# Kernel tuning notes

Measured on AMD Instinct MI355X. Metric: run time of the kernel, lower is better.

## Reference

```python
import jax, jax.numpy as jnp
import numpy as np

NUM_NODE = 90
FEAT_DIM = 32
BATCH = 8192


def setup_inputs() -> dict:
    key = jax.random.key(0)
    k1, k2, k3 = jax.random.split(key, 3)
    sc_feats = jax.random.normal(k1, (BATCH * NUM_NODE, FEAT_DIM), dtype=jnp.float32)
    fc_feats = jax.random.normal(k2, (BATCH * NUM_NODE, FEAT_DIM), dtype=jnp.float32)
    # nn.Linear(feat_dim, feat_dim, bias=False) weight, [out, in]
    W_e = jax.random.normal(k3, (FEAT_DIM, FEAT_DIM), dtype=jnp.float32) * (1.0 / np.sqrt(FEAT_DIM))
    return {"sc_feats": sc_feats, "fc_feats": fc_feats, "W_e": W_e}


def reference(sc_feats, fc_feats, W_e):
    N, D = NUM_NODE, FEAT_DIM
    # exemplar/query: view(-1, N, D) then permute(0,2,1) -> [B, D, N]
    exemplar = sc_feats.reshape(-1, N, D).transpose(0, 2, 1)  # [B, D, N]
    query = fc_feats.reshape(-1, N, D).transpose(0, 2, 1)     # [B, D, N]
    exemplar_t = exemplar.transpose(0, 2, 1)                  # [B, N, D]
    exemplar_corr = jnp.einsum('bnd,ed->bne', exemplar_t, W_e)  # Linear: x @ W^T
    A = jnp.einsum('bnd,bdm->bnm', exemplar_corr, query)      # [B, N, N]
    A1 = jax.nn.softmax(A, axis=1)                            # softmax over dim 1
    Bm = jax.nn.softmax(A.transpose(0, 2, 1), axis=1)         # softmax(A^T, dim=1)
    query_att = jnp.einsum('bdn,bnm->bdm', exemplar, A1)      # [B, D, N]
    exemplar_att = jnp.einsum('bdn,bnm->bdm', query, Bm)      # [B, D, N]
    cosc = query_att.transpose(0, 2, 1).reshape(-1, D)        # [B*N, D]
    cofc = exemplar_att.transpose(0, 2, 1).reshape(-1, D)     # [B*N, D]
    return (cosc, cofc)
```

## Files before the change

### kernel.cpp

```cpp
#include <hip/hip_runtime.h>

typedef __attribute__((ext_vector_type(8))) short short8;
typedef __attribute__((ext_vector_type(4))) short short4v;
typedef __attribute__((ext_vector_type(4))) float f32x4;
typedef __attribute__((ext_vector_type(2))) unsigned uint2v;

#define NN 90
#define FD 32
#define LDE 100
#define LDT 104
#define LOG2E 1.4426950408889634f

__device__ inline unsigned short f2bf(float f) {
  unsigned u = __builtin_bit_cast(unsigned, f);
  return (unsigned short)((u + 0x7fffu + ((u >> 16) & 1u)) >> 16);
}
__device__ inline float bf2f(unsigned short h) {
  unsigned u = ((unsigned)h) << 16;
  return __builtin_bit_cast(float, u);
}
__device__ inline unsigned pk2(float a, float b) {
  unsigned ua = __builtin_bit_cast(unsigned, a);
  unsigned ub = __builtin_bit_cast(unsigned, b);
  return ((ua + 0x7fffu + ((ua >> 16) & 1u)) >> 16) |
         ((ub + 0x7fffu + ((ub >> 16) & 1u)) & 0xFFFF0000u);
}
__device__ inline f32x4 mfma16(short8 a, short8 b, f32x4 c) {
  return __builtin_amdgcn_mfma_f32_16x16x32_bf16(a, b, c, 0, 0, 0);
}
__device__ inline void frag_cvt(f32x4 a, f32x4 b, short8& hi, short8& lo) {
  float v[8] = {a[0], a[1], a[2], a[3], b[0], b[1], b[2], b[3]};
  #pragma unroll
  for (int i = 0; i < 8; ++i) {
    unsigned short h = f2bf(v[i]);
    hi[i] = (short)h;
    lo[i] = (short)(__builtin_bit_cast(unsigned, v[i] - bf2f(h)) >> 16);
  }
}

__global__ __launch_bounds__(256, 5) void CAI_35141422416140_kernel(
    const float* __restrict__ sc, const float* __restrict__ fc,
    const float* __restrict__ we, float* __restrict__ out, int nb)
{
  const int b   = blockIdx.x;
  const int tid = threadIdx.x;
  const int w   = tid >> 6;
  const int l   = tid & 63;
  const int lg  = l >> 4;
  const int lj  = l & 15;

  __shared__ __align__(16) char lds[32512];
  unsigned short* Ghi = (unsigned short*)(lds + 0);
  unsigned short* Glo = (unsigned short*)(lds + 7680);
  unsigned short* E   = (unsigned short*)(lds + 0);
  unsigned short* St  = (unsigned short*)(lds + 19200);
  unsigned short* Ft  = (unsigned short*)(lds + 25856);

  const float* Sg = sc + (size_t)b * (NN * FD);
  const float* Fg = fc + (size_t)b * (NN * FD);

  #pragma unroll
  for (int s = 0; s < 3; ++s) {
    int u  = s * 256 + tid;
    int d  = u & 31;
    int n0 = (u >> 5) * 4;
    float sv[4], fv[4];
    #pragma unroll
    for (int r = 0; r < 4; ++r) {
      bool ok = (n0 + r) < NN;
      sv[r] = ok ? Sg[(n0 + r) * FD + d] : 0.f;
      fv[r] = ok ? Fg[(n0 + r) * FD + d] : 0.f;
    }
    uint2v sp = { pk2(sv[0], sv[1]), pk2(sv[2], sv[3]) };
    uint2v fp = { pk2(fv[0], fv[1]), pk2(fv[2], fv[3]) };
    *(uint2v*)&St[d * LDT + n0] = sp;
    *(uint2v*)&Ft[d * LDT + n0] = fp;
  }

  short8 Wh[2], Wl[2];
  #pragma unroll
  for (int nt = 0; nt < 2; ++nt) {
    #pragma unroll
    for (int e = 0; e < 8; ++e) {
      float wv = we[(lg * 8 + e) * FD + nt * 16 + lj] * LOG2E;
      unsigned short h = f2bf(wv);
      Wh[nt][e] = (short)h;
      Wl[nt][e] = (short)(__builtin_bit_cast(unsigned, wv - bf2f(h)) >> 16);
    }
  }

  #pragma unroll
  for (int rep = 0; rep < 2; ++rep) {
    int mt = w + rep * 4;
    if (mt <= 5) {
      int row = mt * 16 + lj; if (row > NN - 1) row = NN - 1;
      f32x4 f0 = *(const f32x4*)(Fg + row * FD + lg * 8);
      f32x4 f1 = *(const f32x4*)(Fg + row * FD + lg * 8 + 4);
      short8 fh, fl;
      frag_cvt(f0, f1, fh, fl);
      #pragma unroll
      for (int nt = 0; nt < 2; ++nt) {
        f32x4 g = {0.f, 0.f, 0.f, 0.f};
        g = mfma16(fh, Wh[nt], g);
        g = mfma16(fh, Wl[nt], g);
        g = mfma16(fl, Wh[nt], g);
        #pragma unroll
        for (int q = 0; q < 4; ++q) {
          int grow = mt * 16 + lg * 4 + q;
          unsigned short gh = f2bf(g[q]);
          Ghi[grow * 40 + nt * 16 + lj] = gh;
          Glo[grow * 40 + nt * 16 + lj] =
              (unsigned short)(__builtin_bit_cast(unsigned, g[q] - bf2f(gh)) >> 16);
        }
      }
    }
  }
  __syncthreads();

  const int ntq = (w >> 1) * 3, mtq = (w & 1) * 3;
  short8 gh8[3], gl8[3];
  #pragma unroll
  for (int im = 0; im < 3; ++im) {
    gh8[im] = *(const short8*)&Ghi[((mtq + im) * 16 + lj) * 40 + lg * 8];
    gl8[im] = *(const short8*)&Glo[((mtq + im) * 16 + lj) * 40 + lg * 8];
  }
  f32x4 a_acc[9];
  #pragma unroll
  for (int in = 0; in < 3; ++in) {
    int row = (ntq + in) * 16 + lj; if (row > NN - 1) row = NN - 1;
    f32x4 s0 = *(const f32x4*)(Sg + row * FD + lg * 8);
    f32x4 s1 = *(const f32x4*)(Sg + row * FD + lg * 8 + 4);
    short8 sh8, sl8;
    frag_cvt(s0, s1, sh8, sl8);
    #pragma unroll
    for (int im = 0; im < 3; ++im) {
      f32x4 a = {0.f, 0.f, 0.f, 0.f};
      a = mfma16(sh8, gh8[im], a);
      a = mfma16(sh8, gl8[im], a);
      a = mfma16(sl8, gh8[im], a);
      a_acc[in * 3 + im] = a;
    }
  }
  __syncthreads();

  if (tid < 150) {
    uint2v z = {0u, 0u};
    *(uint2v*)(lds + 18000 + tid * 8) = z;
  }
  const unsigned edge_lo = (lg < 3) ? 0xFFFFFFFFu : 0u;
  const unsigned edge_hi = (lg < 2) ? 0xFFFFFFFFu : 0u;
  #pragma unroll
  for (int i = 0; i < 9; ++i) {
    int nt = ntq + i / 3, mt = mtq + i % 3;
    f32x4 a = a_acc[i];
    #pragma unroll
    for (int q = 0; q < 4; ++q) a[q] = __builtin_amdgcn_exp2f(a[q]);
    unsigned a0 = pk2(a[0], a[1]), a1 = pk2(a[2], a[3]);
    if (nt == 5) { a0 &= edge_lo; a1 &= edge_hi; }
    int rowm = mt * 16 + lj;
    if (rowm < NN) {
      uint2v pk = {a0, a1};
      *(uint2v*)&E[rowm * LDE + nt * 16 + lg * 4] = pk;
    }
  }
  __syncthreads();

  const short ONE = (short)0x3F80;
  const short8 ones = {ONE, ONE, ONE, ONE, ONE, ONE, ONE, ONE};
  const size_t ob1 = (size_t)b * (NN * FD);
  const size_t ob2 = (size_t)nb * (NN * FD) + ob1;

  {
    f32x4 inv; int currb = -1;
    #pragma unroll
    for (int i = 0; i < 3; ++i) {
      int t5 = 3 * w + i;
      int rb = t5 >> 1, dt = t5 & 1;
      bool newrb = (rb != currb);
      int arow = rb * 16 + lj; if (arow > NN - 1) arow = NN - 1;
      f32x4 o  = {0.f, 0.f, 0.f, 0.f};
      f32x4 s4 = {0.f, 0.f, 0.f, 0.f};
      #pragma unroll
      for (int ks = 0; ks < 3; ++ks) {
        short4v a0 = *(const short4v*)&E[arow * LDE + ks * 32 + lg * 8];
        short4v a1 = *(const short4v*)&E[arow * LDE + ks * 32 + lg * 8 + 4];
        short8 af = {a0[0], a0[1], a0[2], a0[3], a1[0], a1[1], a1[2], a1[3]};
        short8 bf = *(const short8*)&St[(dt * 16 + lj) * LDT + ks * 32 + lg * 8];
        o = mfma16(af, bf, o);
        if (newrb) s4 = mfma16(af, ones, s4);
      }
      if (newrb) {
        #pragma unroll
        for (int q = 0; q < 4; ++q) inv[q] = __builtin_amdgcn_rcpf(s4[q]);
        currb = rb;
      }
      #pragma unroll
      for (int q = 0; q < 4; ++q) {
        int m = rb * 16 + lg * 4 + q;
        if (m < NN) out[ob1 + m * FD + dt * 16 + lj] = o[q] * inv[q];
      }
    }
  }

  {
    f32x4 inv; int currb = -1;
    #pragma unroll
    for (int i = 0; i < 3; ++i) {
      int t5 = 3 * w + i;
      int rb = t5 >> 1, dt = t5 & 1;
      bool newrb = (rb != currb);
      int acol = rb * 16 + lj;
      f32x4 o  = {0.f, 0.f, 0.f, 0.f};
      f32x4 s4 = {0.f, 0.f, 0.f, 0.f};
      #pragma unroll
      for (int ks = 0; ks < 3; ++ks) {
        short8 af;
        #pragma unroll
        for (int e = 0; e < 8; ++e) {
          int n = ks * 32 + lg * 8 + e;
          af[e] = (short)E[n * LDE + acol];
        }
        short8 bf = *(const short8*)&Ft[(dt * 16 + lj) * LDT + ks * 32 + lg * 8];
        o = mfma16(af, bf, o);
        if (newrb) s4 = mfma16(af, ones, s4);
      }
      if (newrb) {
        #pragma unroll
        for (int q = 0; q < 4; ++q) inv[q] = __builtin_amdgcn_rcpf(s4[q]);
        currb = rb;
      }
      #pragma unroll
      for (int q = 0; q < 4; ++q) {
        int m = rb * 16 + lg * 4 + q;
        if (m < NN) out[ob2 + m * FD + dt * 16 + lj] = o[q] * inv[q];
      }
    }
  }
}

extern "C" void kernel_launch(void* const* d_in, const int* in_sizes, int n_in,
                              void* d_out, int out_size, void* d_ws, size_t ws_size,
                              hipStream_t stream) {
  const float* sc = (const float*)d_in[0];
  const float* fc = (const float*)d_in[1];
  const float* we = (const float*)d_in[2];
  float* out = (float*)d_out;
  int nb = in_sizes[0] / (NN * FD);
  CAI_35141422416140_kernel<<<dim3(nb), dim3(256), 0, stream>>>(sc, fc, we, out, nb);
}
```

Before: 113.4 us.

## Use six waves per block, one 16-row tile per wave

Raises the block from 4 to 6 wavefronts so each wave owns exactly one 16-row tile across all stages: the G projection, the score rows, the exp/store, and both attention outputs. The per-wave loops with irregular tile assignments and the rb-tracking logic go away. The global loads of the wave's own sc/fc rows are hoisted to the top so they overlap the LDS transpose staging. The trade-off is a larger block under launch_bounds(384,8), which tightens the register budget and may change occupancy. The 32 KB of LDS per block may also limit resident blocks.

```diff
diff --git a/kernel.cpp b/kernel.cpp
--- a/kernel.cpp
+++ b/kernel.cpp
@@ -38,7 +38,7 @@
   }
 }
 
-__global__ __launch_bounds__(256, 5) void CAI_35141422416140_kernel(
+__global__ __launch_bounds__(384, 8) void CAI_35141422416140_kernel(
     const float* __restrict__ sc, const float* __restrict__ fc,
     const float* __restrict__ we, float* __restrict__ out, int nb)
 {
@@ -59,9 +59,15 @@
   const float* Sg = sc + (size_t)b * (NN * FD);
   const float* Fg = fc + (size_t)b * (NN * FD);
 
-  #pragma unroll
-  for (int s = 0; s < 3; ++s) {
-    int u  = s * 256 + tid;
+  int row0 = w * 16 + lj; if (row0 > NN - 1) row0 = NN - 1;
+  f32x4 pf0 = *(const f32x4*)(Fg + row0 * FD + lg * 8);
+  f32x4 pf1 = *(const f32x4*)(Fg + row0 * FD + lg * 8 + 4);
+  f32x4 ps0 = *(const f32x4*)(Sg + row0 * FD + lg * 8);
+  f32x4 ps1 = *(const f32x4*)(Sg + row0 * FD + lg * 8 + 4);
+
+  #pragma unroll
+  for (int s = 0; s < 2; ++s) {
+    int u  = s * 384 + tid;
     int d  = u & 31;
     int n0 = (u >> 5) * 4;
     float sv[4], fv[4];
@@ -89,56 +95,40 @@
     }
   }
 
-  #pragma unroll
-  for (int rep = 0; rep < 2; ++rep) {
-    int mt = w + rep * 4;
-    if (mt <= 5) {
-      int row = mt * 16 + lj; if (row > NN - 1) row = NN - 1;
-      f32x4 f0 = *(const f32x4*)(Fg + row * FD + lg * 8);
-      f32x4 f1 = *(const f32x4*)(Fg + row * FD + lg * 8 + 4);
-      short8 fh, fl;
-      frag_cvt(f0, f1, fh, fl);
-      #pragma unroll
-      for (int nt = 0; nt < 2; ++nt) {
-        f32x4 g = {0.f, 0.f, 0.f, 0.f};
-        g = mfma16(fh, Wh[nt], g);
-        g = mfma16(fh, Wl[nt], g);
-        g = mfma16(fl, Wh[nt], g);
-        #pragma unroll
-        for (int q = 0; q < 4; ++q) {
-          int grow = mt * 16 + lg * 4 + q;
-          unsigned short gh = f2bf(g[q]);
-          Ghi[grow * 40 + nt * 16 + lj] = gh;
-          Glo[grow * 40 + nt * 16 + lj] =
-              (unsigned short)(__builtin_bit_cast(unsigned, g[q] - bf2f(gh)) >> 16);
-        }
+  {
+    short8 fh, fl;
+    frag_cvt(pf0, pf1, fh, fl);
+    #pragma unroll
+    for (int nt = 0; nt < 2; ++nt) {
+      f32x4 g = {0.f, 0.f, 0.f, 0.f};
+      g = mfma16(fh, Wh[nt], g);
+      g = mfma16(fh, Wl[nt], g);
+      g = mfma16(fl, Wh[nt], g);
+      #pragma unroll
+      for (int q = 0; q < 4; ++q) {
+        int grow = w * 16 + lg * 4 + q;
+        unsigned short gh = f2bf(g[q]);
+        Ghi[grow * 40 + nt * 16 + lj] = gh;
+        Glo[grow * 40 + nt * 16 + lj] =
+            (unsigned short)(__builtin_bit_cast(unsigned, g[q] - bf2f(gh)) >> 16);
       }
     }
   }
   __syncthreads();
 
-  const int ntq = (w >> 1) * 3, mtq = (w & 1) * 3;
-  short8 gh8[3], gl8[3];
-  #pragma unroll
-  for (int im = 0; im < 3; ++im) {
-    gh8[im] = *(const short8*)&Ghi[((mtq + im) * 16 + lj) * 40 + lg * 8];
-    gl8[im] = *(const short8*)&Glo[((mtq + im) * 16 + lj) * 40 + lg * 8];
-  }
-  f32x4 a_acc[9];
-  #pragma unroll
-  for (int in = 0; in < 3; ++in) {
-    int row = (ntq + in) * 16 + lj; if (row > NN - 1) row = NN - 1;
-    f32x4 s0 = *(const f32x4*)(Sg + row * FD + lg * 8);
-    f32x4 s1 = *(const f32x4*)(Sg + row * FD + lg * 8 + 4);
+  f32x4 acc[6];
+  {
     short8 sh8, sl8;
-    frag_cvt(s0, s1, sh8, sl8);
-    #pragma unroll
-    for (int im = 0; im < 3; ++im) {
+    frag_cvt(ps0, ps1, sh8, sl8);
+    #pragma unroll
+    for (int mt = 0; mt < 6; ++mt) {
+      short8 gh8 = *(const short8*)&Ghi[(mt * 16 + lj) * 40 + lg * 8];
+      short8 gl8 = *(const short8*)&Glo[(mt * 16 + lj) * 40 + lg * 8];
       f32x4 a = {0.f, 0.f, 0.f, 0.f};
-      a = mfma16(sh8, gh8[im], a);
-      a = mfma16(sh8, gl8[im], a);
-      a = mfma16(sl8, gh8[im], a);
-      a_acc[in * 3 + im] = a;
+      a = mfma16(sh8, gh8, a);
+      a = mfma16(sh8, gl8, a);
+      a = mfma16(sl8, gh8, a);
+      acc[mt] = a;
     }
   }
   __syncthreads();
@@ -150,17 +140,16 @@
   const unsigned edge_lo = (lg < 3) ? 0xFFFFFFFFu : 0u;
   const unsigned edge_hi = (lg < 2) ? 0xFFFFFFFFu : 0u;
   #pragma unroll
-  for (int i = 0; i < 9; ++i) {
-    int nt = ntq + i / 3, mt = mtq + i % 3;
-    f32x4 a = a_acc[i];
+  for (int mt = 0; mt < 6; ++mt) {
+    f32x4 a = acc[mt];
     #pragma unroll
     for (int q = 0; q < 4; ++q) a[q] = __builtin_amdgcn_exp2f(a[q]);
     unsigned a0 = pk2(a[0], a[1]), a1 = pk2(a[2], a[3]);
-    if (nt == 5) { a0 &= edge_lo; a1 &= edge_hi; }
+    if (w == 5) { a0 &= edge_lo; a1 &= edge_hi; }
     int rowm = mt * 16 + lj;
     if (rowm < NN) {
       uint2v pk = {a0, a1};
-      *(uint2v*)&E[rowm * LDE + nt * 16 + lg * 4] = pk;
+      *(uint2v*)&E[rowm * LDE + w * 16 + lg * 4] = pk;
     }
   }
   __syncthreads();
@@ -171,13 +160,10 @@
   const size_t ob2 = (size_t)nb * (NN * FD) + ob1;
 
   {
-    f32x4 inv; int currb = -1;
-    #pragma unroll
-    for (int i = 0; i < 3; ++i) {
-      int t5 = 3 * w + i;
-      int rb = t5 >> 1, dt = t5 & 1;
-      bool newrb = (rb != currb);
-      int arow = rb * 16 + lj; if (arow > NN - 1) arow = NN - 1;
+    f32x4 inv;
+    const int arow = w * 16 + lj;
+    #pragma unroll
+    for (int dt = 0; dt < 2; ++dt) {
       f32x4 o  = {0.f, 0.f, 0.f, 0.f};
       f32x4 s4 = {0.f, 0.f, 0.f, 0.f};
       #pragma unroll
@@ -187,29 +173,25 @@
         short8 af = {a0[0], a0[1], a0[2], a0[3], a1[0], a1[1], a1[2], a1[3]};
         short8 bf = *(const short8*)&St[(dt * 16 + lj) * LDT + ks * 32 + lg * 8];
         o = mfma16(af, bf, o);
-        if (newrb) s4 = mfma16(af, ones, s4);
-      }
-      if (newrb) {
+        if (dt == 0) s4 = mfma16(af, ones, s4);
+      }
+      if (dt == 0) {
         #pragma unroll
         for (int q = 0; q < 4; ++q) inv[q] = __builtin_amdgcn_rcpf(s4[q]);
-        currb = rb;
       }
       #pragma unroll
       for (int q = 0; q < 4; ++q) {
-        int m = rb * 16 + lg * 4 + q;
+        int m = w * 16 + lg * 4 + q;
         if (m < NN) out[ob1 + m * FD + dt * 16 + lj] = o[q] * inv[q];
       }
     }
   }
 
   {
-    f32x4 inv; int currb = -1;
-    #pragma unroll
-    for (int i = 0; i < 3; ++i) {
-      int t5 = 3 * w + i;
-      int rb = t5 >> 1, dt = t5 & 1;
-      bool newrb = (rb != currb);
-      int acol = rb * 16 + lj;
+    f32x4 inv;
+    const int acol = w * 16 + lj;
+    #pragma unroll
+    for (int dt = 0; dt < 2; ++dt) {
       f32x4 o  = {0.f, 0.f, 0.f, 0.f};
       f32x4 s4 = {0.f, 0.f, 0.f, 0.f};
       #pragma unroll
@@ -222,16 +204,15 @@
         }
         short8 bf = *(const short8*)&Ft[(dt * 16 + lj) * LDT + ks * 32 + lg * 8];
         o = mfma16(af, bf, o);
-        if (newrb) s4 = mfma16(af, ones, s4);
-      }
-      if (newrb) {
+        if (dt == 0) s4 = mfma16(af, ones, s4);
+      }
+      if (dt == 0) {
         #pragma unroll
         for (int q = 0; q < 4; ++q) inv[q] = __builtin_amdgcn_rcpf(s4[q]);
-        currb = rb;
       }
       #pragma unroll
       for (int q = 0; q < 4; ++q) {
-        int m = rb * 16 + lg * 4 + q;
+        int m = w * 16 + lg * 4 + q;
         if (m < NN) out[ob2 + m * FD + dt * 16 + lj] = o[q] * inv[q];
       }
     }
@@ -246,5 +227,5 @@
   const float* we = (const float*)d_in[2];
   float* out = (float*)d_out;
   int nb = in_sizes[0] / (NN * FD);
-  CAI_35141422416140_kernel<<<dim3(nb), dim3(256), 0, stream>>>(sc, fc, we, out, nb);
-}
+  CAI_35141422416140_kernel<<<dim3(nb), dim3(384), 0, stream>>>(sc, fc, we, out, nb);
+}
```

Result: slower. 121.9 us (+7.5%).
